# Performance work log

Hardware: AMD Instinct MI355X
Metric: run time of the kernel (lower is better)

## Reference

```python
import jax, jax.numpy as jnp
import numpy as np

EPS = 1.1920929e-07  # torch.finfo(float32).eps, used by nn.RMSNorm when eps=None
H = 16  # num_heads


def rmsnorm(x, w):
    return x * jax.lax.rsqrt(jnp.mean(x * x, axis=-1, keepdims=True) + EPS) * w


def attention(x, wq, wk, wv, wo, mask):
    # x: [b, s, d]; mask: [s, s] bool (True = attend)
    b, s, d = x.shape
    hd = d // H
    split = lambda t: t.reshape(b, s, H, hd).transpose(0, 2, 1, 3)  # b h s hd
    q, k, v = split(x @ wq), split(x @ wk), split(x @ wv)
    scale = 1.0 / float(np.sqrt(hd))
    scores = jnp.einsum('bhqd,bhkd->bhqk', q, k) * scale
    scores = jnp.where(mask, scores, jnp.asarray(-1e30, scores.dtype))
    p = jax.nn.softmax(scores, axis=-1)
    o = jnp.einsum('bhqk,bhkd->bhqd', p, v)
    return o.transpose(0, 2, 1, 3).reshape(b, s, d) @ wo


def setup_inputs() -> dict:
    key = jax.random.key(0)
    B, S, D, DFF = 2, 1024, 1024, 4096
    ks = jax.random.split(key, 32)
    w = lambda k, shape: jax.random.normal(k, shape, jnp.float32) * 0.02

    idx = jnp.arange(S)
    col_id = idx % 32            # COLUMN: interleaved column groups
    feat_id = idx // 128         # FEATURE: contiguous feature groups
    col_mask = col_id[:, None] == col_id[None, :]
    feat_mask = feat_id[:, None] == feat_id[None, :]
    nbr_mask = jnp.abs(idx[:, None] - idx[None, :]) <= 64  # NEIGHBOR: local band
    full_mask = jnp.ones((S, S), dtype=bool)

    return {
        'x': jax.random.normal(ks[0], (B, S, D), jnp.float32),
        'col_mask': col_mask, 'feat_mask': feat_mask,
        'nbr_mask': nbr_mask, 'full_mask': full_mask,
        'norm_c': jnp.ones((D,), jnp.float32), 'wq_c': w(ks[1], (D, D)), 'wk_c': w(ks[2], (D, D)), 'wv_c': w(ks[3], (D, D)), 'wo_c': w(ks[4], (D, D)),
        'norm_f': jnp.ones((D,), jnp.float32), 'wq_f': w(ks[5], (D, D)), 'wk_f': w(ks[6], (D, D)), 'wv_f': w(ks[7], (D, D)), 'wo_f': w(ks[8], (D, D)),
        'norm_n': jnp.ones((D,), jnp.float32), 'wq_n': w(ks[9], (D, D)), 'wk_n': w(ks[10], (D, D)), 'wv_n': w(ks[11], (D, D)), 'wo_n': w(ks[12], (D, D)),
        'norm_u': jnp.ones((D,), jnp.float32), 'wq_u': w(ks[13], (D, D)), 'wk_u': w(ks[14], (D, D)), 'wv_u': w(ks[15], (D, D)), 'wo_u': w(ks[16], (D, D)),
        'norm_ffn': jnp.ones((D,), jnp.float32), 'w_up': w(ks[17], (D, DFF)), 'w_gate': w(ks[18], (D, DFF)), 'w_down': w(ks[19], (DFF, D)),
    }


def reference(x, col_mask, feat_mask, nbr_mask, full_mask,
              norm_c, wq_c, wk_c, wv_c, wo_c,
              norm_f, wq_f, wk_f, wv_f, wo_f,
              norm_n, wq_n, wk_n, wv_n, wo_n,
              norm_u, wq_u, wk_u, wv_u, wo_u,
              norm_ffn, w_up, w_gate, w_down):
    x = x + attention(rmsnorm(x, norm_c), wq_c, wk_c, wv_c, wo_c, col_mask)
    x = x + attention(rmsnorm(x, norm_f), wq_f, wk_f, wv_f, wo_f, feat_mask)
    x = x + attention(rmsnorm(x, norm_n), wq_n, wk_n, wv_n, wo_n, nbr_mask)
    x = x + attention(rmsnorm(x, norm_u), wq_u, wk_u, wv_u, wo_u, full_mask)
    h = rmsnorm(x, norm_ffn)
    x = x + (jax.nn.silu(h @ w_gate) * (h @ w_up)) @ w_down  # SwiGLU FFN
    return x
```

## Files before the change

kernel.cpp:

```cpp
#include <hip/hip_runtime.h>
#include <math.h>
#include <stdint.h>


typedef __attribute__((ext_vector_type(8))) short bf16x8;
typedef __attribute__((ext_vector_type(4))) float f32x4;
typedef unsigned short ushort_t;
typedef unsigned int uint_t;

#define DEV static __device__ __forceinline__

DEV float bf2f(ushort_t u) { union { uint_t i; float f; } v; v.i = ((uint_t)u) << 16; return v.f; }
DEV ushort_t f2bf(float f) {
  union { float f; uint_t i; } v; v.f = f;
  uint_t r = v.i + 0x7fffu + ((v.i >> 16) & 1u);
  return (ushort_t)(r >> 16);
}
DEV uint_t pk2(ushort_t a, ushort_t b) { return (uint_t)a | ((uint_t)b << 16); }

DEV void gld16(const ushort_t* g, ushort_t* l) {
  __builtin_amdgcn_global_load_lds((const __attribute__((address_space(1))) void*)g,
                                   (__attribute__((address_space(3))) void*)l, 16, 0, 0);
}

struct Src16 { const float* p[16]; };

__global__ __launch_bounds__(256) void transpose16(Src16 s, ushort_t* __restrict__ qkvT,
                                                   ushort_t* __restrict__ woT) {
  __shared__ float tile[32][33];
  const int mz = blockIdx.z;
  const float* __restrict__ src = s.p[mz];
  const int l = mz >> 2, which = mz & 3;
  ushort_t* dst = (which < 3) ? (qkvT + (size_t)l*3072*1024 + (size_t)which*1024*1024)
                              : (woT  + (size_t)l*1024*1024);
  const int tx = threadIdx.x & 31, ty = threadIdx.x >> 5;
  const int r0 = blockIdx.y*32, c0 = blockIdx.x*32;
#pragma unroll
  for (int i = 0; i < 4; i++) tile[ty + 8*i][tx] = src[(size_t)(r0 + ty + 8*i)*1024 + c0 + tx];
  __syncthreads();
#pragma unroll
  for (int i = 0; i < 4; i++) dst[(size_t)(c0 + ty + 8*i)*1024 + r0 + tx] = f2bf(tile[tx][ty + 8*i]);
}

__global__ __launch_bounds__(256) void transpose_cvt(const float* __restrict__ src,
    ushort_t* __restrict__ dst, int R, int C, int row_off) {
  __shared__ float tile[32][33];
  const int tx = threadIdx.x & 31, ty = threadIdx.x >> 5;
  const int r0 = blockIdx.y*32, c0 = blockIdx.x*32;
#pragma unroll
  for (int i = 0; i < 4; i++) tile[ty + 8*i][tx] = src[(size_t)(r0 + ty + 8*i)*C + c0 + tx];
  __syncthreads();
#pragma unroll
  for (int i = 0; i < 4; i++)
    dst[(size_t)(row_off + c0 + ty + 8*i)*R + r0 + tx] = f2bf(tile[tx][ty + 8*i]);
}

template<int NS, int RMS>
__global__ __launch_bounds__(256) void fused_add_rms(
    const float* __restrict__ resid, const float* __restrict__ Pp,
    const float* __restrict__ w, float* __restrict__ xout,
    ushort_t* __restrict__ xn) {
  const int row = blockIdx.x, t = threadIdx.x;
  const size_t off = (size_t)row*1024 + t*4;
  float4 v = *(const float4*)&resid[off];
#pragma unroll
  for (int s = 0; s < NS; s++) {
    const float4 p = *(const float4*)&Pp[(size_t)s*(2048ull*1024) + off];
    v.x += p.x; v.y += p.y; v.z += p.z; v.w += p.w;
  }
  *(float4*)&xout[off] = v;
  if (RMS) {
    float ss = v.x*v.x + v.y*v.y + v.z*v.z + v.w*v.w;
#pragma unroll
    for (int m = 32; m; m >>= 1) ss += __shfl_xor(ss, m);
    __shared__ float red[4];
    if ((t & 63) == 0) red[t >> 6] = ss;
    __syncthreads();
    const float tot = red[0] + red[1] + red[2] + red[3];
    const float rs = rsqrtf(tot * (1.0f/1024.0f) + 1.1920929e-07f);
    const float4 wv = ((const float4*)w)[t];
    uint2 o;
    o.x = pk2(f2bf(v.x*rs*wv.x), f2bf(v.y*rs*wv.y));
    o.y = pk2(f2bf(v.z*rs*wv.z), f2bf(v.w*rs*wv.w));
    *(uint2*)&xn[off] = o;
  }
}

template<int BM, int BN, int EPI, int SPLITK>
__global__ __launch_bounds__(256, 4) void gemm_bt(
    const ushort_t* __restrict__ A, const ushort_t* __restrict__ BT,
    void* __restrict__ Cout, int M, int N, int K) {
  constexpr int BK = 64;
  __shared__ ushort_t Al[BM*BK];
  __shared__ ushort_t Bl[BN*BK];
  const int t = threadIdx.x, lane = t & 63;
  const int l15 = lane & 15, l4 = lane >> 4;
  int bid = blockIdx.y * gridDim.x + blockIdx.x;
  const int nwg = gridDim.x * gridDim.y;
  if ((nwg & 7) == 0) bid = (bid & 7) * (nwg >> 3) + (bid >> 3);
  const int n0 = (bid % gridDim.x) * BN;
  const int m0 = (bid / gridDim.x) * BM;
  constexpr int WM = BM/2, WN = BN/2, FM = WM/16, FN = WN/16;
  const int wm = ((t >> 6) >> 1) * WM;
  const int wn = ((t >> 6) & 1) * WN;
  const f32x4 zf = {0.f, 0.f, 0.f, 0.f};
  f32x4 acc[FM][FN];
#pragma unroll
  for (int m = 0; m < FM; m++)
#pragma unroll
    for (int n = 0; n < FN; n++) acc[m][n] = zf;
  constexpr int CA = (BM*BK)/(256*8), CB = (BN*BK)/(256*8);
  const int kz = blockIdx.z * (K / SPLITK);
  const int sw = l15 & 7;
  for (int k0 = kz; k0 < kz + K / SPLITK; k0 += BK) {
#pragma unroll
    for (int i = 0; i < CA; i++) {
      const int c = i*256 + t, row = c >> 3, ch = (c & 7) ^ (row & 7);
      gld16(&A[(size_t)(m0 + row)*K + k0 + ch*8], &Al[c*8]);
    }
#pragma unroll
    for (int i = 0; i < CB; i++) {
      const int c = i*256 + t, row = c >> 3, ch = (c & 7) ^ (row & 7);
      gld16(&BT[(size_t)(n0 + row)*K + k0 + ch*8], &Bl[c*8]);
    }
    __syncthreads();
#pragma unroll
    for (int kc = 0; kc < BK; kc += 32) {
      bf16x8 af[FM], bfr[FN];
#pragma unroll
      for (int m = 0; m < FM; m++)
        af[m] = *(const bf16x8*)&Al[(wm + m*16 + l15)*BK + (((kc >> 3) + l4) ^ sw)*8];
#pragma unroll
      for (int n = 0; n < FN; n++)
        bfr[n] = *(const bf16x8*)&Bl[(wn + n*16 + l15)*BK + (((kc >> 3) + l4) ^ sw)*8];
#pragma unroll
      for (int m = 0; m < FM; m++)
#pragma unroll
        for (int n = 0; n < FN; n++)
          acc[m][n] = __builtin_amdgcn_mfma_f32_16x16x32_bf16(af[m], bfr[n], acc[m][n], 0, 0, 0);
    }
    __syncthreads();
  }
#pragma unroll
  for (int m = 0; m < FM; m++)
#pragma unroll
    for (int n = 0; n < FN; n++)
#pragma unroll
      for (int r = 0; r < 4; r++) {
        const int row = m0 + wm + m*16 + l4*4 + r;
        const int col = n0 + wn + n*16 + l15;
        const size_t idx = (size_t)row*N + col;
        const float v = acc[m][n][r];
        if (EPI == 0) ((ushort_t*)Cout)[idx] = f2bf(v);
        else          ((float*)Cout)[(size_t)blockIdx.z*((size_t)M*N) + idx] = v;
      }
}

__global__ __launch_bounds__(256) void attn_col_k(const ushort_t* __restrict__ qkv,
                                                  ushort_t* __restrict__ O) {
  __shared__ float Qs[32][65], Ks[32][65], Vs[32][65], P[32][33];
  const int c = blockIdx.x, h = blockIdx.y, b = blockIdx.z, t = threadIdx.x;
  const size_t base = (size_t)b*1024*3072 + h*64;
  for (int e = t; e < 2048; e += 256) {
    const int u = e >> 6, d = e & 63;
    const size_t rb = base + (size_t)(c + 32*u)*3072 + d;
    Qs[u][d] = bf2f(qkv[rb]);
    Ks[u][d] = bf2f(qkv[rb + 1024]);
    Vs[u][d] = bf2f(qkv[rb + 2048]);
  }
  __syncthreads();
  const int u = t >> 3, kq = (t & 7)*4;
  float sc[4] = {0.f, 0.f, 0.f, 0.f};
  for (int d = 0; d < 64; d++) {
    const float q = Qs[u][d];
#pragma unroll
    for (int j = 0; j < 4; j++) sc[j] += q * Ks[kq + j][d];
  }
#pragma unroll
  for (int j = 0; j < 4; j++) P[u][kq + j] = __expf(sc[j] * 0.125f);
  __syncthreads();
  if (t < 32) {
    float sum = 0.f;
    for (int j = 0; j < 32; j++) sum += P[t][j];
    const float inv = 1.0f / sum;
    for (int j = 0; j < 32; j++) P[t][j] *= inv;
  }
  __syncthreads();
  const int dg = (t & 7)*8;
  float o[8] = {0.f,0.f,0.f,0.f,0.f,0.f,0.f,0.f};
  for (int k = 0; k < 32; k++) {
    const float p = P[u][k];
#pragma unroll
    for (int j = 0; j < 8; j++) o[j] += p * Vs[k][dg + j];
  }
  uint4 w4;
  w4.x = pk2(f2bf(o[0]), f2bf(o[1])); w4.y = pk2(f2bf(o[2]), f2bf(o[3]));
  w4.z = pk2(f2bf(o[4]), f2bf(o[5])); w4.w = pk2(f2bf(o[6]), f2bf(o[7]));
  *(uint4*)&O[(size_t)(b*1024 + c + 32*u)*1024 + h*64 + dg] = w4;
}

template<int MASK, int NSPLIT>
__global__ __launch_bounds__(256, 4) void attn_flash_k(const ushort_t* __restrict__ qkv,
    ushort_t* __restrict__ O, float* __restrict__ Opart, float* __restrict__ Lpart) {
  constexpr int LP = 66;
  __shared__ ushort_t Kl[64*LP];
  __shared__ ushort_t Vt[64*LP];
  __shared__ ushort_t Pl[4][16*LP];
  const int t = threadIdx.x, lane = t & 63, wave = t >> 6;
  const int l15 = lane & 15, l4 = lane >> 4;
  const int qt = blockIdx.x, h = blockIdx.y;
  const int b = blockIdx.z / NSPLIT, sp = blockIdx.z % NSPLIT;
  const int q0 = qt*64;
  const size_t base = (size_t)b*1024*3072 + h*64;
  const int qrow = q0 + wave*16 + l15;
  const bf16x8 qf0 = *(const bf16x8*)&qkv[base + (size_t)qrow*3072 + l4*8];
  const bf16x8 qf1 = *(const bf16x8*)&qkv[base + (size_t)qrow*3072 + 32 + l4*8];
  int klo, khi;
  if (MASK == 0)      { klo = q0 & ~127; khi = klo + 128; }
  else if (MASK == 1) { klo = (q0 >= 64) ? q0 - 64 : 0; khi = (q0 + 128 < 1024) ? q0 + 128 : 1024; }
  else                { klo = sp * (1024/NSPLIT); khi = klo + 1024/NSPLIT; }
  const int kr = t >> 2, kd = (t & 3)*16;
  const int vk2 = (t & 31)*2, vd = (t >> 5)*8;
  const ushort_t* kptr = qkv + base + 1024 + (size_t)kr*3072 + kd;
  const ushort_t* vptr = qkv + base + 2048 + (size_t)vk2*3072 + vd;
  bf16x8 kg0 = *(const bf16x8*)&kptr[(size_t)klo*3072];
  bf16x8 kg1 = *(const bf16x8*)&kptr[(size_t)klo*3072 + 8];
  bf16x8 vg0 = *(const bf16x8*)&vptr[(size_t)klo*3072];
  bf16x8 vg1 = *(const bf16x8*)&vptr[(size_t)klo*3072 + 3072];
  const f32x4 zf = {0.f, 0.f, 0.f, 0.f};
  f32x4 of[4];
#pragma unroll
  for (int n = 0; n < 4; n++) of[n] = zf;
  float lrow[4] = {0.f, 0.f, 0.f, 0.f};

  for (int kb = klo; kb < khi; kb += 64) {
    *(bf16x8*)&Kl[kr*LP + kd] = kg0;
    *(bf16x8*)&Kl[kr*LP + kd + 8] = kg1;
#pragma unroll
    for (int j = 0; j < 8; j++)
      *(uint_t*)&Vt[(vd + j)*LP + vk2] = pk2((ushort_t)vg0[j], (ushort_t)vg1[j]);
    __syncthreads();
    if (kb + 64 < khi) {
      kg0 = *(const bf16x8*)&kptr[(size_t)(kb+64)*3072];
      kg1 = *(const bf16x8*)&kptr[(size_t)(kb+64)*3072 + 8];
      vg0 = *(const bf16x8*)&vptr[(size_t)(kb+64)*3072];
      vg1 = *(const bf16x8*)&vptr[(size_t)(kb+64)*3072 + 3072];
    }
    f32x4 sf[4];
    __builtin_amdgcn_s_setprio(1);
#pragma unroll
    for (int s = 0; s < 4; s++) {
      const bf16x8 k0 = *(const bf16x8*)&Kl[(s*16 + l15)*LP + l4*8];
      const bf16x8 k1 = *(const bf16x8*)&Kl[(s*16 + l15)*LP + 32 + l4*8];
      sf[s] = __builtin_amdgcn_mfma_f32_16x16x32_bf16(qf0, k0, zf, 0, 0, 0);
      sf[s] = __builtin_amdgcn_mfma_f32_16x16x32_bf16(qf1, k1, sf[s], 0, 0, 0);
    }
    __builtin_amdgcn_s_setprio(0);
    float psum[4] = {0.f, 0.f, 0.f, 0.f};
#pragma unroll
    for (int s = 0; s < 4; s++)
#pragma unroll
      for (int r = 0; r < 4; r++) {
        float a = sf[s][r]*0.125f;
        if (MASK == 1) {
          const int d = (q0 + wave*16 + l4*4 + r) - (kb + s*16 + l15);
          if (d > 64 || d < -64) a = -1e30f;
        }
        const float p = __expf(a);
        psum[r] += p;
        Pl[wave][(l4*4 + r)*LP + s*16 + l15] = f2bf(p);
      }
#pragma unroll
    for (int mk = 1; mk < 16; mk <<= 1)
#pragma unroll
      for (int r = 0; r < 4; r++) psum[r] += __shfl_xor(psum[r], mk);
#pragma unroll
    for (int r = 0; r < 4; r++) lrow[r] += psum[r];
    const bf16x8 pa0 = *(const bf16x8*)&Pl[wave][l15*LP + l4*8];
    const bf16x8 pa1 = *(const bf16x8*)&Pl[wave][l15*LP + 32 + l4*8];
    __builtin_amdgcn_s_setprio(1);
#pragma unroll
    for (int n = 0; n < 4; n++) {
      const bf16x8 v0 = *(const bf16x8*)&Vt[(n*16 + l15)*LP + l4*8];
      const bf16x8 v1 = *(const bf16x8*)&Vt[(n*16 + l15)*LP + 32 + l4*8];
      of[n] = __builtin_amdgcn_mfma_f32_16x16x32_bf16(pa0, v0, of[n], 0, 0, 0);
      of[n] = __builtin_amdgcn_mfma_f32_16x16x32_bf16(pa1, v1, of[n], 0, 0, 0);
    }
    __builtin_amdgcn_s_setprio(0);
    __syncthreads();
  }
  if (NSPLIT == 1) {
#pragma unroll
    for (int n = 0; n < 4; n++)
#pragma unroll
      for (int r = 0; r < 4; r++) {
        const int qg = q0 + wave*16 + l4*4 + r;
        O[(size_t)(b*1024 + qg)*1024 + h*64 + n*16 + l15] = f2bf(of[n][r] / lrow[r]);
      }
  } else {
#pragma unroll
    for (int r = 0; r < 4; r++) {
      const int qg = q0 + wave*16 + l4*4 + r;
      const size_t row = ((size_t)(sp*2 + b)*1024 + qg)*16 + h;
#pragma unroll
      for (int n = 0; n < 4; n++) Opart[row*64 + n*16 + l15] = of[n][r];
      if (l15 == 0) Lpart[row] = lrow[r];
    }
  }
}

template<int NS>
__global__ __launch_bounds__(256) void attn_merge_k(const float* __restrict__ Opart,
    const float* __restrict__ L, ushort_t* __restrict__ O) {
  const int idx = blockIdx.x*256 + threadIdx.x;
  const int d8 = (idx & 7)*8;
  const int h  = (idx >> 3) & 15;
  const int q  = (idx >> 7) & 1023;
  const int b  = idx >> 17;
  float den = 0.f;
  float acc[8] = {0,0,0,0,0,0,0,0};
#pragma unroll
  for (int s = 0; s < NS; s++) {
    const size_t row = ((size_t)(s*2 + b)*1024 + q)*16 + h;
    den += L[row];
    const float4* op = (const float4*)&Opart[row*64 + d8];
    const float4 a = op[0], c = op[1];
    acc[0] += a.x; acc[1] += a.y; acc[2] += a.z; acc[3] += a.w;
    acc[4] += c.x; acc[5] += c.y; acc[6] += c.z; acc[7] += c.w;
  }
  const float inv = 1.0f / den;
  uint4 w4;
  w4.x = pk2(f2bf(acc[0]*inv), f2bf(acc[1]*inv));
  w4.y = pk2(f2bf(acc[2]*inv), f2bf(acc[3]*inv));
  w4.z = pk2(f2bf(acc[4]*inv), f2bf(acc[5]*inv));
  w4.w = pk2(f2bf(acc[6]*inv), f2bf(acc[7]*inv));
  *(uint4*)&O[((size_t)b*1024 + q)*1024 + h*64 + d8] = w4;
}

__global__ __launch_bounds__(256) void swiglu_k(const ushort_t* __restrict__ gu,
                                                ushort_t* __restrict__ out) {
  const size_t idx = (size_t)blockIdx.x*256 + threadIdx.x;
  const size_t m = idx >> 9, j8 = (idx & 511) << 3;
  const bf16x8 g8 = *(const bf16x8*)&gu[m*8192 + j8];
  const bf16x8 u8 = *(const bf16x8*)&gu[m*8192 + 4096 + j8];
  ushort_t o[8];
#pragma unroll
  for (int i = 0; i < 8; i++) {
    const float g = bf2f((ushort_t)g8[i]);
    const float u = bf2f((ushort_t)u8[i]);
    o[i] = f2bf(u * g / (1.0f + __expf(-g)));
  }
  uint4 w4;
  w4.x = pk2(o[0], o[1]); w4.y = pk2(o[2], o[3]); w4.z = pk2(o[4], o[5]); w4.w = pk2(o[6], o[7]);
  *(uint4*)&out[m*4096 + j8] = w4;
}

extern "C" void kernel_launch(void* const* d_in, const int* in_sizes, int n_in,
                              void* d_out, int out_size, void* d_ws, size_t ws_size,
                              hipStream_t stream) {
  (void)in_sizes; (void)n_in; (void)out_size; (void)ws_size;
  const float* x_in = (const float*)d_in[0];
  const float* norm[5] = { (const float*)d_in[5], (const float*)d_in[10], (const float*)d_in[15],
                           (const float*)d_in[20], (const float*)d_in[25] };
  char* w = (char*)d_ws;
  auto alloc = [&](size_t bytes) { char* p = w; w += (bytes + 255) & ~(size_t)255; return p; };
  ushort_t* qkvT = (ushort_t*)alloc(4ull*3072*1024*2);
  ushort_t* woT  = (ushort_t*)alloc(4ull*1024*1024*2);
  ushort_t* guT  = (ushort_t*)alloc(8192ull*1024*2);
  ushort_t* dnT  = (ushort_t*)alloc(4096ull*1024*2);
  float*    xbuf = (float*)  alloc(2048ull*1024*4);
  ushort_t* xn   = (ushort_t*)alloc(2048ull*1024*2);
  ushort_t* qkv  = (ushort_t*)alloc(2048ull*3072*2);
  ushort_t* attO = (ushort_t*)alloc(2048ull*1024*2);
  ushort_t* gu   = (ushort_t*)alloc(2048ull*8192*2);
  ushort_t* hmid = (ushort_t*)alloc(2048ull*4096*2);
  float* Pp    = (float*)gu;
  float* Opart = (float*)gu;
  float* Lpart = (float*)hmid;

  Src16 s;
  for (int l = 0; l < 4; l++) {
    s.p[l*4 + 0] = (const float*)d_in[6 + l*5];
    s.p[l*4 + 1] = (const float*)d_in[7 + l*5];
    s.p[l*4 + 2] = (const float*)d_in[8 + l*5];
    s.p[l*4 + 3] = (const float*)d_in[9 + l*5];
  }
  transpose16<<<dim3(32, 32, 16), 256, 0, stream>>>(s, qkvT, woT);
  transpose_cvt<<<dim3(128, 32), 256, 0, stream>>>((const float*)d_in[27], guT, 1024, 4096, 0);
  transpose_cvt<<<dim3(128, 32), 256, 0, stream>>>((const float*)d_in[26], guT, 1024, 4096, 4096);
  transpose_cvt<<<dim3(32, 128), 256, 0, stream>>>((const float*)d_in[28], dnT, 4096, 1024, 0);

  fused_add_rms<0,1><<<2048, 256, 0, stream>>>(x_in, nullptr, norm[0], xbuf, xn);

  for (int l = 0; l < 4; l++) {
    gemm_bt<64,128,0,1><<<dim3(3072/128, 2048/64), 256, 0, stream>>>(
        xn, qkvT + (size_t)l*3072*1024, qkv, 2048, 3072, 1024);
    if (l == 0)      attn_col_k         <<<dim3(32, 16, 2), 256, 0, stream>>>(qkv, attO);
    else if (l == 1) attn_flash_k<0,1>  <<<dim3(16, 16, 2), 256, 0, stream>>>(qkv, attO, nullptr, nullptr);
    else if (l == 2) attn_flash_k<1,1>  <<<dim3(16, 16, 2), 256, 0, stream>>>(qkv, attO, nullptr, nullptr);
    else {
      attn_flash_k<2,4><<<dim3(16, 16, 8), 256, 0, stream>>>(qkv, nullptr, Opart, Lpart);
      attn_merge_k<4><<<1024, 256, 0, stream>>>(Opart, Lpart, attO);
    }
    gemm_bt<128,64,3,2><<<dim3(1024/64, 2048/128, 2), 256, 0, stream>>>(
        attO, woT + (size_t)l*1024*1024, Pp, 2048, 1024, 1024);
    fused_add_rms<2,1><<<2048, 256, 0, stream>>>(xbuf, Pp, norm[l+1 < 4 ? l+1 : 4], xbuf, xn);
  }
  gemm_bt<128,128,0,1><<<dim3(8192/128, 2048/128), 256, 0, stream>>>(xn, guT, gu, 2048, 8192, 1024);
  swiglu_k<<<4096, 256, 0, stream>>>(gu, hmid);
  gemm_bt<128,128,3,4><<<dim3(1024/128, 2048/128, 4), 256, 0, stream>>>(
      hmid, dnT, Pp, 2048, 1024, 4096);
  fused_add_rms<4,0><<<2048, 256, 0, stream>>>(xbuf, Pp, nullptr, (float*)d_out, nullptr);
}
```

Before: 534.3 us.

## Fuse gate/up GEMM with SwiGLU epilogue and retile QKV GEMM

Replaces the separate gate/up GEMM plus SwiGLU elementwise kernel with one GEMM that accumulates gate and up tiles side by side and applies SiLU(g)*u in the epilogue. This removes the 2048x8192 bf16 intermediate write and re-read and one launch. The fused kernel holds 32 accumulator tiles per wave, so register pressure is high and occupancy may drop. The QKV projection GEMM tile width also changes from 128 to 192 columns, and attention scratch moves to a dedicated buffer because the gu buffer is gone.

```diff
diff --git a/kernel.cpp b/kernel.cpp
--- a/kernel.cpp
+++ b/kernel.cpp
@@ -153,6 +153,71 @@
         const float v = acc[m][n][r];
         if (EPI == 0) ((ushort_t*)Cout)[idx] = f2bf(v);
         else          ((float*)Cout)[(size_t)blockIdx.z*((size_t)M*N) + idx] = v;
+      }
+}
+
+__global__ __launch_bounds__(256, 2) void gemm_gu_swiglu(
+    const ushort_t* __restrict__ A, const ushort_t* __restrict__ BT,
+    ushort_t* __restrict__ H) {
+  constexpr int BK = 64;
+  __shared__ ushort_t Al[128*BK];
+  __shared__ ushort_t Bg[128*BK];
+  __shared__ ushort_t Bu[128*BK];
+  const int t = threadIdx.x, lane = t & 63;
+  const int l15 = lane & 15, l4 = lane >> 4;
+  int bid = blockIdx.y * gridDim.x + blockIdx.x;
+  const int nwg = gridDim.x * gridDim.y;
+  bid = (bid & 7) * (nwg >> 3) + (bid >> 3);
+  const int n0 = (bid % gridDim.x) * 128;
+  const int m0 = (bid / gridDim.x) * 128;
+  const int wm = ((t >> 6) >> 1) * 64;
+  const int wn = ((t >> 6) & 1) * 64;
+  const f32x4 zf = {0.f, 0.f, 0.f, 0.f};
+  f32x4 ag[4][4], au[4][4];
+#pragma unroll
+  for (int m = 0; m < 4; m++)
+#pragma unroll
+    for (int n = 0; n < 4; n++) { ag[m][n] = zf; au[m][n] = zf; }
+  const int sw = l15 & 7;
+  for (int k0 = 0; k0 < 1024; k0 += BK) {
+#pragma unroll
+    for (int i = 0; i < 4; i++) {
+      const int c = i*256 + t, row = c >> 3, ch = (c & 7) ^ (row & 7);
+      gld16(&A [(size_t)(m0 + row)*1024 + k0 + ch*8], &Al[c*8]);
+      gld16(&BT[(size_t)(n0 + row)*1024 + k0 + ch*8], &Bg[c*8]);
+      gld16(&BT[(size_t)(4096 + n0 + row)*1024 + k0 + ch*8], &Bu[c*8]);
+    }
+    __syncthreads();
+#pragma unroll
+    for (int kc = 0; kc < BK; kc += 32) {
+      const int co = (((kc >> 3) + l4) ^ sw)*8;
+      bf16x8 af[4], bgf[4], buf_[4];
+#pragma unroll
+      for (int m = 0; m < 4; m++) af[m]   = *(const bf16x8*)&Al[(wm + m*16 + l15)*BK + co];
+#pragma unroll
+      for (int n = 0; n < 4; n++) bgf[n]  = *(const bf16x8*)&Bg[(wn + n*16 + l15)*BK + co];
+#pragma unroll
+      for (int n = 0; n < 4; n++) buf_[n] = *(const bf16x8*)&Bu[(wn + n*16 + l15)*BK + co];
+#pragma unroll
+      for (int m = 0; m < 4; m++)
+#pragma unroll
+        for (int n = 0; n < 4; n++) {
+          ag[m][n] = __builtin_amdgcn_mfma_f32_16x16x32_bf16(af[m], bgf[n], ag[m][n], 0, 0, 0);
+          au[m][n] = __builtin_amdgcn_mfma_f32_16x16x32_bf16(af[m], buf_[n], au[m][n], 0, 0, 0);
+        }
+    }
+    __syncthreads();
+  }
+#pragma unroll
+  for (int m = 0; m < 4; m++)
+#pragma unroll
+    for (int n = 0; n < 4; n++)
+#pragma unroll
+      for (int r = 0; r < 4; r++) {
+        const int row = m0 + wm + m*16 + l4*4 + r;
+        const int col = n0 + wn + n*16 + l15;
+        const float g = ag[m][n][r], u = au[m][n][r];
+        H[(size_t)row*4096 + col] = f2bf(u * g / (1.0f + __expf(-g)));
       }
 }
 
@@ -337,24 +402,6 @@
   *(uint4*)&O[((size_t)b*1024 + q)*1024 + h*64 + d8] = w4;
 }
 
-__global__ __launch_bounds__(256) void swiglu_k(const ushort_t* __restrict__ gu,
-                                                ushort_t* __restrict__ out) {
-  const size_t idx = (size_t)blockIdx.x*256 + threadIdx.x;
-  const size_t m = idx >> 9, j8 = (idx & 511) << 3;
-  const bf16x8 g8 = *(const bf16x8*)&gu[m*8192 + j8];
-  const bf16x8 u8 = *(const bf16x8*)&gu[m*8192 + 4096 + j8];
-  ushort_t o[8];
-#pragma unroll
-  for (int i = 0; i < 8; i++) {
-    const float g = bf2f((ushort_t)g8[i]);
-    const float u = bf2f((ushort_t)u8[i]);
-    o[i] = f2bf(u * g / (1.0f + __expf(-g)));
-  }
-  uint4 w4;
-  w4.x = pk2(o[0], o[1]); w4.y = pk2(o[2], o[3]); w4.z = pk2(o[4], o[5]); w4.w = pk2(o[6], o[7]);
-  *(uint4*)&out[m*4096 + j8] = w4;
-}
-
 extern "C" void kernel_launch(void* const* d_in, const int* in_sizes, int n_in,
                               void* d_out, int out_size, void* d_ws, size_t ws_size,
                               hipStream_t stream) {
@@ -372,10 +419,10 @@
   ushort_t* xn   = (ushort_t*)alloc(2048ull*1024*2);
   ushort_t* qkv  = (ushort_t*)alloc(2048ull*3072*2);
   ushort_t* attO = (ushort_t*)alloc(2048ull*1024*2);
-  ushort_t* gu   = (ushort_t*)alloc(2048ull*8192*2);
   ushort_t* hmid = (ushort_t*)alloc(2048ull*4096*2);
-  float* Pp    = (float*)gu;
-  float* Opart = (float*)gu;
+  float*  scratch = (float*)alloc(8ull*1024*16*64*4);
+  float* Pp    = scratch;
+  float* Opart = scratch;
   float* Lpart = (float*)hmid;
 
   Src16 s;
@@ -393,7 +440,7 @@
   fused_add_rms<0,1><<<2048, 256, 0, stream>>>(x_in, nullptr, norm[0], xbuf, xn);
 
   for (int l = 0; l < 4; l++) {
-    gemm_bt<64,128,0,1><<<dim3(3072/128, 2048/64), 256, 0, stream>>>(
+    gemm_bt<64,192,0,1><<<dim3(3072/192, 2048/64), 256, 0, stream>>>(
         xn, qkvT + (size_t)l*3072*1024, qkv, 2048, 3072, 1024);
     if (l == 0)      attn_col_k         <<<dim3(32, 16, 2), 256, 0, stream>>>(qkv, attO);
     else if (l == 1) attn_flash_k<0,1>  <<<dim3(16, 16, 2), 256, 0, stream>>>(qkv, attO, nullptr, nullptr);
@@ -406,8 +453,7 @@
         attO, woT + (size_t)l*1024*1024, Pp, 2048, 1024, 1024);
     fused_add_rms<2,1><<<2048, 256, 0, stream>>>(xbuf, Pp, norm[l+1 < 4 ? l+1 : 4], xbuf, xn);
   }
-  gemm_bt<128,128,0,1><<<dim3(8192/128, 2048/128), 256, 0, stream>>>(xn, guT, gu, 2048, 8192, 1024);
-  swiglu_k<<<4096, 256, 0, stream>>>(gu, hmid);
+  gemm_gu_swiglu<<<dim3(4096/128, 2048/128), 256, 0, stream>>>(xn, guT, hmid);
   gemm_bt<128,128,3,4><<<dim3(1024/128, 2048/128, 4), 256, 0, stream>>>(
       hmid, dnT, Pp, 2048, 1024, 4096);
   fused_add_rms<4,0><<<2048, 256, 0, stream>>>(xbuf, Pp, nullptr, (float*)d_out, nullptr);
```

After: 506.5 us. 1.05x faster.
